# Optimization experiments

Measured on AMD Instinct MI355X. Metric: run time of the kernel, lower is better.

The kernel has to match this reference:

```python
import jax, jax.numpy as jnp
import numpy as np
import math

B, S, HID = 2, 2048, 2048
NH, HD = 16, HID // 16          # num_heads, head_dim
RING = 4
CH = S // RING                  # chunk size per ring rank
SEG_LEN = 2048                  # segment_lengths[0]
DIL = 2                         # dilation_rates[0]


def setup_inputs() -> dict:
    key = jax.random.key(0)
    k1, k2, k3 = jax.random.split(key, 3)
    x = jax.random.normal(k1, (B, S, HID), dtype=jnp.float32)
    # Linear weights stored input-major so y = x @ W (same math as torch x @ W.T)
    W_qkv = jax.random.normal(k2, (HID, 3 * HID), dtype=jnp.float32) * 0.02
    W_out = jax.random.normal(k3, (HID, HID), dtype=jnp.float32) * 0.02
    return {"x": x, "W_qkv": W_qkv, "W_out": W_out}


def _dilated_mask():
    # mask[i, j] = (segment(i) == segment(j)) and (|i - j| % DIL == 0)
    pos = jnp.arange(S)
    seg = pos // SEG_LEN
    same_seg = seg[:, None] == seg[None, :]
    dil_ok = (jnp.abs(pos[:, None] - pos[None, :]) % DIL) == 0
    return same_seg & dil_ok  # [S, S] bool


def reference(x, W_qkv, W_out):
    qkv = (x @ W_qkv).reshape(B, S, 3, NH, HD)
    q, k, v = jnp.moveaxis(qkv, 2, 0)          # each [B, S, NH, HD]
    q = jnp.transpose(q, (0, 2, 1, 3))          # [B, NH, S, HD]
    k = jnp.transpose(k, (0, 2, 1, 3))
    v = jnp.transpose(v, (0, 2, 1, 3))

    scores = jnp.einsum('bhqd,bhkd->bhqk', q, k) / math.sqrt(HD)  # [B,NH,S,S]
    if DIL > 1:
        scores = jnp.where(_dilated_mask()[None, None], scores, -jnp.inf)

    # Reshape into (q-chunk, kv-chunk) blocks to reproduce the per-chunk
    # (non-rescaled) softmax of the ring loop: each kv chunk subtracts its OWN
    # max, exps, and the un-rescaled numerators/denominators are summed.
    s = scores.reshape(B, NH, RING, CH, RING, CH)        # [B,H,Rq,Cq,Rk,Ck]
    m = jnp.max(s, axis=-1, keepdims=True)               # per-kv-chunk row max
    e = jnp.exp(s - m)                                   # -inf -> 0
    v_ch = v.reshape(B, NH, RING, CH, HD)                # [B,H,Rk,Ck,HD]
    num = jnp.einsum('bhqcrk,bhrkd->bhqcd', e, v_ch)     # [B,H,Rq,Cq,HD]
    den = jnp.sum(e, axis=(-2, -1))[..., None]           # [B,H,Rq,Cq,1]
    out = num / (den + 1e-8)

    out = out.reshape(B, NH, S, HD)
    out = jnp.transpose(out, (0, 2, 1, 3)).reshape(B, S, HID)
    return out @ W_out
```

## Files before the change

kernel.cpp:

```cpp
#include <hip/hip_runtime.h>
#include <stdint.h>

typedef float  f32x4  __attribute__((ext_vector_type(4)));
typedef __bf16 bf16x8 __attribute__((ext_vector_type(8)));

#define AS1 __attribute__((address_space(1)))
#define AS3 __attribute__((address_space(3)))


__global__ void k_cvt_x_blk(const float* __restrict__ x, __bf16* __restrict__ y) {
  const int d = blockIdx.x * 256 + threadIdx.x;
  const int row = d & 127, kg = (d >> 7) & 3, mbkt = d >> 9;
  const int mb = mbkt & 31, kt = mbkt >> 5;
  const int m = mb * 128 + row, k0 = kt * 32 + kg * 8;
  const float4 v0 = *reinterpret_cast<const float4*>(x + (size_t)m * 2048 + k0);
  const float4 v1 = *reinterpret_cast<const float4*>(x + (size_t)m * 2048 + k0 + 4);
  bf16x8 o;
  o[0] = (__bf16)v0.x; o[1] = (__bf16)v0.y; o[2] = (__bf16)v0.z; o[3] = (__bf16)v0.w;
  o[4] = (__bf16)v1.x; o[5] = (__bf16)v1.y; o[6] = (__bf16)v1.z; o[7] = (__bf16)v1.w;
  *reinterpret_cast<bf16x8*>(y + (size_t)d * 8) = o;
}

__global__ void k_cvt_wt_blk(const float* __restrict__ w, __bf16* __restrict__ wt,
                             const int N, const int NBK) {
  __shared__ float tile[64][65];
  const int k0 = blockIdx.x * 64, n0 = blockIdx.y * 64;
  const int t = threadIdx.x;
  #pragma unroll
  for (int i = 0; i < 16; ++i) {
    const int idx = t + 256 * i;
    const int r = idx >> 6, c = idx & 63;
    tile[r][c] = w[(size_t)(k0 + r) * N + n0 + c];
  }
  __syncthreads();
  #pragma unroll
  for (int i = 0; i < 2; ++i) {
    const int v = t + 256 * i;
    const int kb = v >> 6, nn = v & 63;
    const int n = n0 + nn, k = k0 + kb * 8;
    bf16x8 o;
    #pragma unroll
    for (int j = 0; j < 8; ++j) o[j] = (__bf16)tile[kb * 8 + j][nn];
    const size_t dst = ((size_t)(k >> 5) * NBK + (n >> 7)) * 4096 +
                       (size_t)((k >> 3) & 3) * 1024 + (n & 127) * 8;
    *reinterpret_cast<bf16x8*>(wt + dst) = o;
  }
}

template<int NBB, int CHK, int EPI>
__global__ __launch_bounds__(256, 3) void k_gemm_r8(
    const __bf16* __restrict__ Ab, const __bf16* __restrict__ Bb,
    __bf16* __restrict__ Oq, __bf16* __restrict__ Ok, __bf16* __restrict__ Ov,
    float* __restrict__ Of) {
  __shared__ __bf16 As[3][4096];
  __shared__ __bf16 Bs[3][4096];
  const int tid = threadIdx.x;
  const int w = tid >> 6, l = tid & 63, g = l >> 4, l15 = l & 15;
  const int wr = w >> 1, wc = w & 1;
  const int bx = blockIdx.x;
  const int wid = (bx & 7) * CHK + (bx >> 3);
  const int nb = wid % NBB, mb = wid / NBB;
  const size_t Abase = (size_t)mb * 4096, Bbase = (size_t)nb * 4096;
  const size_t Astep = (size_t)32 * 4096, Bstep = (size_t)NBB * 4096;
  const int soff = w * 1024;

  f32x4 acc[4][4] = {};

  auto STAGE = [&](int t, int b) {
    const __bf16* as_ = Ab + (size_t)t * Astep + Abase + soff + l * 8;
    const __bf16* bs_ = Bb + (size_t)t * Bstep + Bbase + soff + l * 8;
    __builtin_amdgcn_global_load_lds((const AS1 uint32_t*)as_,
                                     (AS3 uint32_t*)(&As[b][soff]), 16, 0, 0);
    __builtin_amdgcn_global_load_lds((const AS1 uint32_t*)(as_ + 512),
                                     (AS3 uint32_t*)(&As[b][soff + 512]), 16, 0, 0);
    __builtin_amdgcn_global_load_lds((const AS1 uint32_t*)bs_,
                                     (AS3 uint32_t*)(&Bs[b][soff]), 16, 0, 0);
    __builtin_amdgcn_global_load_lds((const AS1 uint32_t*)(bs_ + 512),
                                     (AS3 uint32_t*)(&Bs[b][soff + 512]), 16, 0, 0);
  };

  STAGE(0, 0);
  STAGE(1, 1);
  asm volatile("s_waitcnt vmcnt(4)" ::: "memory");
  __builtin_amdgcn_s_barrier();

  int cur = 0;
  for (int t = 0; t < 64; ++t) {
    int b2 = cur + 2; if (b2 >= 3) b2 -= 3;
    if (t + 2 < 64) STAGE(t + 2, b2);
    const __bf16* Ar = &As[cur][g * 1024 + (wr * 64 + l15) * 8];
    const __bf16* Br = &Bs[cur][g * 1024 + (wc * 64 + l15) * 8];
    bf16x8 af[4], bfr[4];
    #pragma unroll
    for (int mi = 0; mi < 4; ++mi) af[mi] = *reinterpret_cast<const bf16x8*>(Ar + mi * 128);
    #pragma unroll
    for (int ni = 0; ni < 4; ++ni) bfr[ni] = *reinterpret_cast<const bf16x8*>(Br + ni * 128);
    __builtin_amdgcn_s_setprio(1);
    #pragma unroll
    for (int mi = 0; mi < 4; ++mi)
      #pragma unroll
      for (int ni = 0; ni < 4; ++ni)
        acc[mi][ni] = __builtin_amdgcn_mfma_f32_16x16x32_bf16(af[mi], bfr[ni], acc[mi][ni], 0, 0, 0);
    __builtin_amdgcn_s_setprio(0);
    __builtin_amdgcn_sched_barrier(0);
    if (t < 62) asm volatile("s_waitcnt vmcnt(4)" ::: "memory");
    else        asm volatile("s_waitcnt vmcnt(0)" ::: "memory");
    __builtin_amdgcn_s_barrier();
    cur = cur + 1; if (cur >= 3) cur -= 3;
  }

  if constexpr (EPI == 1) {
    const int m0 = mb * 128, n0 = nb * 128;
    const int ty = n0 >> 11;
    const int h = (n0 & 2047) >> 7;
    #pragma unroll
    for (int mi = 0; mi < 4; ++mi) {
      #pragma unroll
      for (int r = 0; r < 4; ++r) {
        const int m = m0 + wr * 64 + mi * 16 + 4 * g + r;
        const int s = m & 2047;
        const int sp = s & 1, s2 = s >> 1;
        const int bb = m >> 11;
        const size_t base = ((((size_t)bb * 16 + h) * 2 + sp) << 17);
        #pragma unroll
        for (int ni = 0; ni < 4; ++ni) {
          const int d = wc * 64 + ni * 16 + l15;
          const __bf16 v = (__bf16)acc[mi][ni][r];
          if (ty == 0)      Oq[base + (size_t)s2 * 128 + d] = v;
          else if (ty == 1) Ok[base + (size_t)s2 * 128 + d] = v;
          else              Ov[base + (size_t)d * 1024 + s2] = v;
        }
      }
    }
  } else {
    #pragma unroll
    for (int mi = 0; mi < 4; ++mi)
      #pragma unroll
      for (int r = 0; r < 4; ++r) {
        const int m = mb * 128 + wr * 64 + mi * 16 + 4 * g + r;
        #pragma unroll
        for (int ni = 0; ni < 4; ++ni) {
          const int n = nb * 128 + wc * 64 + ni * 16 + l15;
          Of[(size_t)m * 2048 + n] = acc[mi][ni][r];
        }
      }
  }
}

__global__ __launch_bounds__(256, 2) void k_attn(
    const __bf16* __restrict__ Qp, const __bf16* __restrict__ Kp,
    const __bf16* __restrict__ Vt, __bf16* __restrict__ attnA) {
  __shared__ __bf16 Ks[64 * 128];
  __shared__ __bf16 Vs[128 * 64];
  __shared__ __bf16 E[4][16][136];

  const int bx = blockIdx.x;
  const int wid = (bx & 7) * 128 + (bx >> 3);
  const int qt = wid & 15, p = (wid >> 4) & 1, h = (wid >> 5) & 15, b = wid >> 9;
  const int tid = threadIdx.x;
  const int w = tid >> 6, l = tid & 63, g = l >> 4, l15 = l & 15;
  const size_t base = ((((size_t)b * 16 + h) * 2 + p) << 17);
  const __bf16* Qb = Qp + base;
  const __bf16* Kb = Kp + base;
  const __bf16* Vb = Vt + base;
  const int q0 = qt * 64 + w * 16;
  const float SC = 1.4426950408889634f / 11.313708498984761f;

  bf16x8 qf[4];
  #pragma unroll
  for (int ks = 0; ks < 4; ++ks)
    qf[ks] = *reinterpret_cast<const bf16x8*>(Qb + (size_t)(q0 + l15) * 128 + ks * 32 + 8 * g);

  f32x4 num[8] = {};
  float den[4] = {0.f, 0.f, 0.f, 0.f};

  const int krow_in = l >> 4;
  const int vrow_in = l >> 3;
  const int vsrc_e = (((l & 7) * 16) ^ (vrow_in << 4)) >> 1;

  for (int c = 0; c < 4; ++c) {
    f32x4 s[16] = {};
    #pragma unroll
    for (int st = 0; st < 4; ++st) {
      __syncthreads();
      #pragma unroll
      for (int i = 0; i < 4; ++i) {
        const int ch = w * 4 + i;
        const int row = ch * 4 + krow_in;
        const int cb = (l15 * 16) ^ ((row & 7) << 4);
        const __bf16* src = Kb + (size_t)(c * 256 + st * 64 + row) * 128 + (cb >> 1);
        __builtin_amdgcn_global_load_lds((const AS1 uint32_t*)src,
                                         (AS3 uint32_t*)(Ks + ch * 512), 16, 0, 0);
      }
      __syncthreads();
      #pragma unroll
      for (int ks = 0; ks < 4; ++ks) {
        #pragma unroll
        for (int nf2 = 0; nf2 < 4; ++nf2) {
          const int r = nf2 * 16 + l15;
          const int cb = (ks * 64 + g * 16) ^ ((r & 7) << 4);
          const bf16x8 kf = *reinterpret_cast<const bf16x8*>(Ks + r * 128 + (cb >> 1));
          s[st * 4 + nf2] = __builtin_amdgcn_mfma_f32_16x16x32_bf16(qf[ks], kf, s[st * 4 + nf2], 0, 0, 0);
        }
      }
    }
    float mv[4];
    #pragma unroll
    for (int r = 0; r < 4; ++r) {
      float m0v = s[0][r];
      #pragma unroll
      for (int nf = 1; nf < 16; ++nf) m0v = fmaxf(m0v, s[nf][r]);
      m0v = fmaxf(m0v, __shfl_xor(m0v, 1));
      m0v = fmaxf(m0v, __shfl_xor(m0v, 2));
      m0v = fmaxf(m0v, __shfl_xor(m0v, 4));
      m0v = fmaxf(m0v, __shfl_xor(m0v, 8));
      mv[r] = m0v;
    }
    #pragma unroll
    for (int r = 0; r < 4; ++r) {
      float ds = 0.f;
      #pragma unroll
      for (int nf = 0; nf < 16; ++nf) {
        const float e = exp2f((s[nf][r] - mv[r]) * SC);
        s[nf][r] = e;
        ds += e;
      }
      den[r] += ds;
    }
    #pragma unroll
    for (int h2 = 0; h2 < 2; ++h2) {
      #pragma unroll
      for (int nf = 0; nf < 8; ++nf)
        #pragma unroll
        for (int r = 0; r < 4; ++r)
          E[w][4 * g + r][nf * 16 + l15] = (__bf16)s[h2 * 8 + nf][r];
      #pragma unroll
      for (int sv = 0; sv < 2; ++sv) {
        const int kv0 = c * 256 + h2 * 128 + sv * 64;
        __syncthreads();
        #pragma unroll
        for (int i = 0; i < 4; ++i) {
          const int ch = w * 4 + i;
          const int row = ch * 8 + vrow_in;
          const __bf16* src = Vb + (size_t)row * 1024 + kv0 + vsrc_e;
          __builtin_amdgcn_global_load_lds((const AS1 uint32_t*)src,
                                           (AS3 uint32_t*)(Vs + ch * 512), 16, 0, 0);
        }
        __syncthreads();
        #pragma unroll
        for (int ks2 = 0; ks2 < 2; ++ks2) {
          const bf16x8 a = *reinterpret_cast<const bf16x8*>(
              &E[w][l15][sv * 64 + ks2 * 32 + 8 * g]);
          #pragma unroll
          for (int nd = 0; nd < 8; ++nd) {
            const int d = nd * 16 + l15;
            const int cb = (ks2 * 64 + g * 16) ^ ((d & 7) << 4);
            const bf16x8 vf = *reinterpret_cast<const bf16x8*>(Vs + d * 64 + (cb >> 1));
            num[nd] = __builtin_amdgcn_mfma_f32_16x16x32_bf16(a, vf, num[nd], 0, 0, 0);
          }
        }
      }
    }
  }

  #pragma unroll
  for (int r = 0; r < 4; ++r) {
    den[r] += __shfl_xor(den[r], 1);
    den[r] += __shfl_xor(den[r], 2);
    den[r] += __shfl_xor(den[r], 4);
    den[r] += __shfl_xor(den[r], 8);
    den[r] += 1e-8f;
  }

  #pragma unroll
  for (int nd = 0; nd < 8; ++nd)
    #pragma unroll
    for (int r = 0; r < 4; ++r) {
      const int sq = q0 + 4 * g + r;
      const int srow = 2 * sq + p;
      const int m = b * 2048 + srow;
      const int k = h * 128 + nd * 16 + l15;
      const size_t dst = ((size_t)(k >> 5) * 32 + (m >> 7)) * 4096 +
                         (size_t)((k >> 3) & 3) * 1024 + (m & 127) * 8 + (k & 7);
      attnA[dst] = (__bf16)(num[nd][r] / den[r]);
    }
}

extern "C" void kernel_launch(void* const* d_in, const int* in_sizes, int n_in,
                              void* d_out, int out_size, void* d_ws, size_t ws_size,
                              hipStream_t stream) {
  (void)in_sizes; (void)n_in; (void)out_size; (void)ws_size;
  const float* x    = (const float*)d_in[0];
  const float* wqkv = (const float*)d_in[1];
  const float* wout = (const float*)d_in[2];
  float* out = (float*)d_out;
  uint8_t* ws = (uint8_t*)d_ws;

  __bf16* xbf   = (__bf16*)(ws + 0);
  __bf16* wqkvt = (__bf16*)(ws + (16ull << 20));
  __bf16* woutt = (__bf16*)(ws + (40ull << 20));
  __bf16* Qp    = (__bf16*)(ws + (48ull << 20));
  __bf16* Kp    = (__bf16*)(ws + (64ull << 20));
  __bf16* Vt    = (__bf16*)(ws + (80ull << 20));
  __bf16* attnA = (__bf16*)(ws + 0);

  k_cvt_x_blk<<<4096, 256, 0, stream>>>(x, xbf);
  k_cvt_wt_blk<<<dim3(32, 96), 256, 0, stream>>>(wqkv, wqkvt, 6144, 48);
  k_cvt_wt_blk<<<dim3(32, 32), 256, 0, stream>>>(wout, woutt, 2048, 16);
  k_gemm_r8<48, 192, 1><<<1536, 256, 0, stream>>>(xbf, wqkvt, Qp, Kp, Vt, nullptr);
  k_attn<<<1024, 256, 0, stream>>>(Qp, Kp, Vt, attnA);
  k_gemm_r8<16, 64, 2><<<512, 256, 0, stream>>>(attnA, woutt, nullptr, nullptr, nullptr, out);
}
```

Before: 281.6 us.

## Triple-buffer K/V tiles with async LDS prefetch two stages ahead in attention

Replaces the separate K and V shared buffers with a unified three-slot ring and sequences all 32 K/V load phases as one pipeline, issuing each load two phases before it is consumed. The double __syncthreads per tile is replaced by vmcnt waits plus a single barrier per phase, and MFMA sections are raised to high priority with s_setprio. This aims to hide global-to-LDS latency behind matrix math, at the cost of more LDS per block (48KB plus the E buffer), which may limit occupancy at two blocks per CU. It also relies on hand-counted vmcnt values being correct.

```diff
diff --git a/kernel.cpp b/kernel.cpp
--- a/kernel.cpp
+++ b/kernel.cpp
@@ -150,59 +150,92 @@
 __global__ __launch_bounds__(256, 2) void k_attn(
     const __bf16* __restrict__ Qp, const __bf16* __restrict__ Kp,
     const __bf16* __restrict__ Vt, __bf16* __restrict__ attnA) {
-  __shared__ __bf16 Ks[64 * 128];
-  __shared__ __bf16 Vs[128 * 64];
+  __shared__ __bf16 U[3][8192];
   __shared__ __bf16 E[4][16][136];
 
   const int bx = blockIdx.x;
   const int wid = (bx & 7) * 128 + (bx >> 3);
-  const int qt = wid & 15, p = (wid >> 4) & 1, h = (wid >> 5) & 15, b = wid >> 9;
+  const int qt = wid & 15, pp = (wid >> 4) & 1, h = (wid >> 5) & 15, b = wid >> 9;
   const int tid = threadIdx.x;
   const int w = tid >> 6, l = tid & 63, g = l >> 4, l15 = l & 15;
-  const size_t base = ((((size_t)b * 16 + h) * 2 + p) << 17);
+  const size_t base = ((((size_t)b * 16 + h) * 2 + pp) << 17);
   const __bf16* Qb = Qp + base;
   const __bf16* Kb = Kp + base;
   const __bf16* Vb = Vt + base;
   const int q0 = qt * 64 + w * 16;
   const float SC = 1.4426950408889634f / 11.313708498984761f;
 
-  bf16x8 qf[4];
-  #pragma unroll
-  for (int ks = 0; ks < 4; ++ks)
-    qf[ks] = *reinterpret_cast<const bf16x8*>(Qb + (size_t)(q0 + l15) * 128 + ks * 32 + 8 * g);
-
-  f32x4 num[8] = {};
-  float den[4] = {0.f, 0.f, 0.f, 0.f};
-
   const int krow_in = l >> 4;
   const int vrow_in = l >> 3;
   const int vsrc_e = (((l & 7) * 16) ^ (vrow_in << 4)) >> 1;
 
-  for (int c = 0; c < 4; ++c) {
-    f32x4 s[16] = {};
-    #pragma unroll
-    for (int st = 0; st < 4; ++st) {
-      __syncthreads();
+  bf16x8 qf[4];
+  #pragma unroll
+  for (int ks = 0; ks < 4; ++ks)
+    qf[ks] = *reinterpret_cast<const bf16x8*>(Qb + (size_t)(q0 + l15) * 128 + ks * 32 + 8 * g);
+
+  f32x4 num[8] = {};
+  float den[4] = {0.f, 0.f, 0.f, 0.f};
+  f32x4 s[16];
+
+  auto STAGE = [&](int p) {
+    const int c = p >> 3, j = p & 7, bi = p % 3;
+    if (j < 4) {
       #pragma unroll
       for (int i = 0; i < 4; ++i) {
         const int ch = w * 4 + i;
         const int row = ch * 4 + krow_in;
         const int cb = (l15 * 16) ^ ((row & 7) << 4);
-        const __bf16* src = Kb + (size_t)(c * 256 + st * 64 + row) * 128 + (cb >> 1);
+        const __bf16* src = Kb + (size_t)(c * 256 + j * 64 + row) * 128 + (cb >> 1);
         __builtin_amdgcn_global_load_lds((const AS1 uint32_t*)src,
-                                         (AS3 uint32_t*)(Ks + ch * 512), 16, 0, 0);
-      }
-      __syncthreads();
+                                         (AS3 uint32_t*)(&U[bi][ch * 512]), 16, 0, 0);
+      }
+    } else {
+      const int kv0 = c * 256 + ((j - 4) >> 1) * 128 + ((j - 4) & 1) * 64;
+      #pragma unroll
+      for (int i = 0; i < 4; ++i) {
+        const int ch = w * 4 + i;
+        const int row = ch * 8 + vrow_in;
+        const __bf16* src = Vb + (size_t)row * 1024 + kv0 + vsrc_e;
+        __builtin_amdgcn_global_load_lds((const AS1 uint32_t*)src,
+                                         (AS3 uint32_t*)(&U[bi][ch * 512]), 16, 0, 0);
+      }
+    }
+  };
+  auto ENDPHASE = [&](int p) {
+    if (p <= 29)      asm volatile("s_waitcnt vmcnt(4)" ::: "memory");
+    else if (p == 30) asm volatile("s_waitcnt vmcnt(0)" ::: "memory");
+    if (p < 31) __builtin_amdgcn_s_barrier();
+  };
+
+  STAGE(0);
+  STAGE(1);
+  asm volatile("s_waitcnt vmcnt(4)" ::: "memory");
+  __builtin_amdgcn_s_barrier();
+
+  for (int c = 0; c < 4; ++c) {
+    const int pb = 8 * c;
+    #pragma unroll
+    for (int i = 0; i < 16; ++i) s[i] = f32x4{0.f, 0.f, 0.f, 0.f};
+    #pragma unroll
+    for (int st = 0; st < 4; ++st) {
+      const int p = pb + st;
+      if (p + 2 < 32) STAGE(p + 2);
+      const __bf16* Kbuf = U[p % 3];
+      __builtin_amdgcn_s_setprio(1);
       #pragma unroll
       for (int ks = 0; ks < 4; ++ks) {
         #pragma unroll
         for (int nf2 = 0; nf2 < 4; ++nf2) {
           const int r = nf2 * 16 + l15;
           const int cb = (ks * 64 + g * 16) ^ ((r & 7) << 4);
-          const bf16x8 kf = *reinterpret_cast<const bf16x8*>(Ks + r * 128 + (cb >> 1));
+          const bf16x8 kf = *reinterpret_cast<const bf16x8*>(Kbuf + r * 128 + (cb >> 1));
           s[st * 4 + nf2] = __builtin_amdgcn_mfma_f32_16x16x32_bf16(qf[ks], kf, s[st * 4 + nf2], 0, 0, 0);
         }
       }
+      __builtin_amdgcn_s_setprio(0);
+      __builtin_amdgcn_sched_barrier(0);
+      ENDPHASE(p);
     }
     float mv[4];
     #pragma unroll
@@ -236,29 +269,25 @@
           E[w][4 * g + r][nf * 16 + l15] = (__bf16)s[h2 * 8 + nf][r];
       #pragma unroll
       for (int sv = 0; sv < 2; ++sv) {
-        const int kv0 = c * 256 + h2 * 128 + sv * 64;
-        __syncthreads();
-        #pragma unroll
-        for (int i = 0; i < 4; ++i) {
-          const int ch = w * 4 + i;
-          const int row = ch * 8 + vrow_in;
-          const __bf16* src = Vb + (size_t)row * 1024 + kv0 + vsrc_e;
-          __builtin_amdgcn_global_load_lds((const AS1 uint32_t*)src,
-                                           (AS3 uint32_t*)(Vs + ch * 512), 16, 0, 0);
-        }
-        __syncthreads();
+        const int p = pb + 4 + h2 * 2 + sv;
+        if (p + 2 < 32) STAGE(p + 2);
+        const __bf16* Vbuf = U[p % 3];
+        __builtin_amdgcn_s_setprio(1);
         #pragma unroll
         for (int ks2 = 0; ks2 < 2; ++ks2) {
           const bf16x8 a = *reinterpret_cast<const bf16x8*>(
-              &E[w][l15][sv * 64 + ks2 * 32 + 8 * g]);
+              &E[w][l15][h2 * 0 + sv * 64 + ks2 * 32 + 8 * g]);
           #pragma unroll
           for (int nd = 0; nd < 8; ++nd) {
             const int d = nd * 16 + l15;
             const int cb = (ks2 * 64 + g * 16) ^ ((d & 7) << 4);
-            const bf16x8 vf = *reinterpret_cast<const bf16x8*>(Vs + d * 64 + (cb >> 1));
+            const bf16x8 vf = *reinterpret_cast<const bf16x8*>(Vbuf + d * 64 + (cb >> 1));
             num[nd] = __builtin_amdgcn_mfma_f32_16x16x32_bf16(a, vf, num[nd], 0, 0, 0);
           }
         }
+        __builtin_amdgcn_s_setprio(0);
+        __builtin_amdgcn_sched_barrier(0);
+        ENDPHASE(p);
       }
     }
   }
@@ -277,7 +306,7 @@
     #pragma unroll
     for (int r = 0; r < 4; ++r) {
       const int sq = q0 + 4 * g + r;
-      const int srow = 2 * sq + p;
+      const int srow = 2 * sq + pp;
       const int m = b * 2048 + srow;
       const int k = h * 128 + nd * 16 + l15;
       const size_t dst = ((size_t)(k >> 5) * 32 + (m >> 7)) * 4096 +
```

Result: no change. 276.2 us (-1.9%).
